# Performance work log

Measured on AMD Instinct MI355X. Metric: run time of the kernel, lower is better.

Reference implementation:

```python
import jax, jax.numpy as jnp
import numpy as np
import itertools

N = 2048
E = 2
B = 8
MAX_ORDERS = (3, 2)
FS = (8, 64, N)  # fs[-1] must equal N for the final Linear (as in the torch code)


def _term_matrices(gsos: np.ndarray, max_order: int) -> np.ndarray:
    """All multigraph polynomial terms S_{i1} @ ... @ S_{id}, d = 1..max_order.
    gsos: [E, N, N] -> returns [T, N, N] with T = E + E^2 + ... + E^max_order."""
    terms = []
    for length in range(1, max_order + 1):
        for idxs in itertools.product(range(gsos.shape[0]), repeat=length):
            m = gsos[idxs[0]]
            for j in idxs[1:]:
                m = m @ gsos[j]
            terms.append(m)
    return np.stack(terms, axis=0)


def setup_inputs() -> dict:
    rng = np.random.default_rng(0)
    # scale so products of up to 3 GSOs stay bounded (op-norm of randn/sqrt(N) ~ 2)
    gsos = (rng.standard_normal((E, N, N)) / (2.0 * np.sqrt(N))).astype(np.float32)
    terms1 = jnp.asarray(_term_matrices(gsos, MAX_ORDERS[0]))  # [14, N, N]
    terms2 = jnp.asarray(_term_matrices(gsos, MAX_ORDERS[1]))  # [6,  N, N]

    key = jax.random.key(0)
    k_x, k_w1, k_w2, k_lin = jax.random.split(key, 4)
    x = jax.random.normal(k_x, (B, FS[0], N), dtype=jnp.float32)
    # torch init: normal(mean=0.05, std=0.01); f_edge dim (=1) squeezed
    w1 = 0.05 + 0.01 * jax.random.normal(k_w1, (FS[1], terms1.shape[0] + 1, FS[0]), dtype=jnp.float32)
    b1 = jnp.zeros((FS[1], 1), dtype=jnp.float32)
    w2 = 0.05 + 0.01 * jax.random.normal(k_w2, (FS[2], terms2.shape[0] + 1, FS[1]), dtype=jnp.float32)
    b2 = jnp.zeros((FS[2], 1), dtype=jnp.float32)
    w_lin = jax.random.normal(k_lin, (2, N), dtype=jnp.float32) / np.sqrt(N)
    b_lin = jnp.zeros((2,), dtype=jnp.float32)
    return dict(x=x, terms1=terms1, terms2=terms2, w1=w1, b1=b1, w2=w2, b2=b2,
                w_lin=w_lin, b_lin=b_lin)


def _mg_filter(x, terms, w, b):
    """MultiGraphFilter forward (f_edge=1 squeezed).
    x: [B,G,N], terms: [T,N,N], w: [F,T+1,G], b: [F,1] -> [B,F,N].
    Equivalent to the torch repeat+matmul+cat+contract, without replication."""
    xS = jnp.einsum('bgm,tmn->btgn', x, terms)          # diffusion for every term
    z = jnp.concatenate([x[:, None], xS], axis=1)        # [B, K=T+1, G, N] (k=0 identity)
    return jnp.einsum('bkgn,fkg->bfn', z, w) + b         # combine + bias


def reference(x, terms1, terms2, w1, b1, w2, b2, w_lin, b_lin):
    h = jax.nn.sigmoid(_mg_filter(x, terms1, w1, b1))    # [B, 64,  N]
    h = jax.nn.sigmoid(_mg_filter(h, terms2, w2, b2))    # [B, N,   N]
    # torch nn.Linear(fs[-1]=N, 2) acts on the last (node) dim
    y = jax.nn.sigmoid(jnp.einsum('bfn,on->bfo', h, w_lin) + b_lin)  # [B, N, 2]
    return jnp.abs(y)
```

## Files before the change

kernel.cpp:

```cpp
#include <hip/hip_runtime.h>

typedef __attribute__((ext_vector_type(8))) short short8;
typedef __attribute__((ext_vector_type(4))) float f32x4;
typedef __attribute__((ext_vector_type(4))) unsigned short u16x4;

#define NN 2048
#define KG2 448
#define NK1 15
#define NG1 8
#define NF1 64
#define SLICE (2048L * 2048L)
#define XSL (64L * 2048L)
#define HSL (512L * 2048L)

static __device__ __forceinline__ unsigned short f2bf(float v) {
    union { float f; unsigned int u; } a; a.f = v;
    unsigned int u = a.u;
    u += 0x7fffu + ((u >> 16) & 1u);
    return (unsigned short)(u >> 16);
}
static __device__ __forceinline__ float bf2f(unsigned short s) {
    union { float f; unsigned int u; } a; a.u = ((unsigned int)s) << 16;
    return a.f;
}
static __device__ __forceinline__ float sigmoidf_(float v) {
    return 1.f / (1.f + __expf(-v));
}
template <int N> static __device__ __forceinline__ void waitvm() {
    asm volatile("s_waitcnt vmcnt(%0)" ::"n"(N) : "memory");
}
template <int LPT> static __device__ __forceinline__ void waitrem(int rem) {
    if (rem >= 3) waitvm<3 * LPT>();
    else if (rem == 2) waitvm<2 * LPT>();
    else if (rem == 1) waitvm<1 * LPT>();
    else waitvm<0>();
}

template <int BM, int BN, int PIPE>
static __device__ __forceinline__ void gemm_core(
    const unsigned short* __restrict__ Ap, int lda,
    const unsigned short* __restrict__ Bp, int ldb, int K,
    unsigned short* Alds, unsigned short* Blds,
    f32x4 (&acc)[BM / 32][BN / 32], int tid) {
    constexpr int MI = BM / 32, NI = BN / 32;
    constexpr int ACH = BM / 64, BCH = BN / 64;
    constexpr int LPT = ACH + BCH;
    const int lane = tid & 63;
    const int wv = tid >> 6;
    const int q = lane >> 4, r = lane & 15;
    const int wm = (wv >> 1) * (BM / 2), wn = (wv & 1) * (BN / 2);

    auto stage = [&](int k0, int buf) {
        unsigned short* Ab = Alds + buf * (BM * 32);
        unsigned short* Bb = Blds + buf * (BN * 32);
#pragma unroll
        for (int c = 0; c < ACH; ++c) {
            const int row = (tid >> 2) + c * 64;
            const unsigned short* gp = Ap + (long)row * lda + k0 + (tid & 3) * 8;
            char* lb = (char*)Ab + c * 4096 + wv * 1024;
            __builtin_amdgcn_global_load_lds(
                (const __attribute__((address_space(1))) void*)gp,
                (__attribute__((address_space(3))) void*)lb, 16, 0, 0);
        }
#pragma unroll
        for (int c = 0; c < BCH; ++c) {
            const int row = (tid >> 2) + c * 64;
            const unsigned short* gp = Bp + (long)row * ldb + k0 + (tid & 3) * 8;
            char* lb = (char*)Bb + c * 4096 + wv * 1024;
            __builtin_amdgcn_global_load_lds(
                (const __attribute__((address_space(1))) void*)gp,
                (__attribute__((address_space(3))) void*)lb, 16, 0, 0);
        }
    };
    auto compute = [&](int buf) {
        const unsigned short* Ab = Alds + buf * (BM * 32);
        const unsigned short* Bb = Blds + buf * (BN * 32);
        short8 af[MI], bfv[NI];
#pragma unroll
        for (int i = 0; i < MI; ++i)
            af[i] = *(const short8*)&Ab[(wm + i * 16 + r) * 32 + q * 8];
#pragma unroll
        for (int j = 0; j < NI; ++j)
            bfv[j] = *(const short8*)&Bb[(wn + j * 16 + r) * 32 + q * 8];
#pragma unroll
        for (int i = 0; i < MI; ++i)
#pragma unroll
            for (int j = 0; j < NI; ++j)
                acc[i][j] = __builtin_amdgcn_mfma_f32_16x16x32_bf16(
                    af[i], bfv[j], acc[i][j], 0, 0, 0);
    };

    const int NT = K >> 5;
    if constexpr (PIPE == 1) {
        for (int t = 0; t < NT; ++t) {
            stage(t * 32, 0);
            __syncthreads();
            compute(0);
            __syncthreads();
        }
    } else {
#pragma unroll
        for (int p = 0; p < PIPE - 1; ++p)
            if (p < NT) stage(p * 32, p);
        for (int t = 0; t < NT; ++t) {
            if (t + PIPE - 1 < NT)
                stage((t + PIPE - 1) * 32, (t + PIPE - 1) & (PIPE - 1));
            int rem = NT - 1 - t;
            if (rem > PIPE - 1) rem = PIPE - 1;
            waitrem<LPT>(rem);
            __builtin_amdgcn_s_barrier();
            compute(t & (PIPE - 1));
            __builtin_amdgcn_s_barrier();
        }
    }
}

template <int BM, int BN>
static __device__ __forceinline__ void epi_bf16(
    f32x4 (&acc)[BM / 32][BN / 32], unsigned short* dst, int ld, int tid) {
    const int lane = tid & 63, wv = tid >> 6, q = lane >> 4, r = lane & 15;
    const int wm = (wv >> 1) * (BM / 2), wn = (wv & 1) * (BN / 2);
#pragma unroll
    for (int i = 0; i < BM / 32; ++i)
#pragma unroll
        for (int j = 0; j < BN / 32; ++j)
#pragma unroll
            for (int e = 0; e < 4; ++e)
                dst[(long)(wm + i * 16 + q * 4 + e) * ld + wn + j * 16 + r] =
                    f2bf(acc[i][j][e]);
}

template <int BM, int BN>
static __device__ __forceinline__ void epi_z2t(
    f32x4 (&acc)[BM / 32][BN / 32], unsigned short* z2t,
    int m0, int n0, int kidx, int tid) {
    const int lane = tid & 63, wv = tid >> 6, q = lane >> 4, r = lane & 15;
    const int wm = (wv >> 1) * (BM / 2), wn = (wv & 1) * (BN / 2);
#pragma unroll
    for (int i = 0; i < BM / 32; ++i)
#pragma unroll
        for (int j = 0; j < BN / 32; ++j) {
            const int row0 = m0 + wm + i * 16 + q * 4;
            const int bb = row0 >> 6, gg = row0 & 63;
            const int col = n0 + wn + j * 16 + r;
            u16x4 pk;
            pk[0] = f2bf(acc[i][j][0]); pk[1] = f2bf(acc[i][j][1]);
            pk[2] = f2bf(acc[i][j][2]); pk[3] = f2bf(acc[i][j][3]);
            *(u16x4*)&z2t[((long)bb * NN + col) * KG2 + kidx * 64 + gg] = pk;
        }
}

__global__ __launch_bounds__(256) void prep_k(const float* __restrict__ S,
                                              const float* __restrict__ x,
                                              unsigned short* __restrict__ St,
                                              unsigned short* __restrict__ xbf) {
    if (blockIdx.z < 2) {
        __shared__ float t[32][33];
        const int e = blockIdx.z;
        const int n0 = blockIdx.x * 32, k0 = blockIdx.y * 32;
        const int tx = threadIdx.x & 31, ty = threadIdx.x >> 5;
        const float* src = S + (long)e * SLICE;
        unsigned short* dst = St + (long)e * SLICE;
#pragma unroll
        for (int i = 0; i < 4; ++i)
            t[ty + i * 8][tx] = src[(long)(k0 + ty + i * 8) * NN + n0 + tx];
        __syncthreads();
#pragma unroll
        for (int i = 0; i < 4; ++i)
            dst[(long)(n0 + ty + i * 8) * NN + k0 + tx] = f2bf(t[tx][ty + i * 8]);
    } else {
        const long i = (long)(blockIdx.y * 64 + blockIdx.x) * 256 + threadIdx.x;
        if (i < 131072L) xbf[i] = f2bf(x[i]);
    }
}

template <int PIPE>
__global__ __launch_bounds__(256) void g1_k(const unsigned short* __restrict__ A,
                                            long a_bstride, int a_shr,
                                            const unsigned short* __restrict__ St,
                                            unsigned short* __restrict__ outp) {
    __shared__ __attribute__((aligned(16))) unsigned short smem[PIPE * 128 * 32];
    const int tid = threadIdx.x;
    const int n0 = blockIdx.x * 64;
    const int z = blockIdx.z;
    const unsigned short* Ap = A + (long)(z >> a_shr) * a_bstride;
    const unsigned short* Bp = St + (long)(z & 1) * SLICE + (long)n0 * NN;

    f32x4 acc[2][2];
#pragma unroll
    for (int i = 0; i < 2; ++i)
#pragma unroll
        for (int j = 0; j < 2; ++j) acc[i][j] = (f32x4){0.f, 0.f, 0.f, 0.f};
    gemm_core<64, 64, PIPE>(Ap, NN, Bp, NN, NN, smem, smem + PIPE * 64 * 32,
                            acc, tid);
    epi_bf16<64, 64>(acc, outp + (long)z * XSL + n0, NN, tid);
}

template <int PIPE, bool CHAIN>
__global__ __launch_bounds__(256) void g2_k(const unsigned short* __restrict__ A,
                                            long a_bstride, int a_shr,
                                            const unsigned short* __restrict__ St,
                                            unsigned short* __restrict__ z2t,
                                            int kbase,
                                            unsigned short* __restrict__ chain) {
    __shared__ __attribute__((aligned(16))) unsigned short smem[PIPE * 192 * 32];
    const int tid = threadIdx.x;
    const int n0 = blockIdx.x * 128;
    const int m0 = blockIdx.y * 64;
    const int z = blockIdx.z;
    const unsigned short* Ap = A + (long)(z >> a_shr) * a_bstride + (long)m0 * NN;
    const unsigned short* Bp = St + (long)(z & 1) * SLICE + (long)n0 * NN;

    f32x4 acc[2][4];
#pragma unroll
    for (int i = 0; i < 2; ++i)
#pragma unroll
        for (int j = 0; j < 4; ++j) acc[i][j] = (f32x4){0.f, 0.f, 0.f, 0.f};
    gemm_core<64, 128, PIPE>(Ap, NN, Bp, NN, NN, smem, smem + PIPE * 64 * 32,
                             acc, tid);
    epi_z2t<64, 128>(acc, z2t, m0, n0, kbase + z, tid);
    if (CHAIN)
        epi_bf16<64, 128>(acc, chain + (long)z * HSL + (long)m0 * NN + n0, NN, tid);
}

__global__ __launch_bounds__(256) void combine1_k(const float* __restrict__ x,
                                                  const unsigned short* __restrict__ xSbf,
                                                  const float* __restrict__ w1,
                                                  const float* __restrict__ b1,
                                                  const float* __restrict__ w2,
                                                  unsigned short* __restrict__ A2,
                                                  unsigned short* __restrict__ z2t,
                                                  unsigned short* __restrict__ w2bf) {
    const int tid = threadIdx.x;
    if (blockIdx.y >= 8) {
        const int sb = (blockIdx.y - 8) * 16 + blockIdx.x;
        for (long i4 = (long)sb * 256 + tid; i4 < 229376L; i4 += 32768L) {
            const float4 v = *(const float4*)&w2[i4 * 4];
            u16x4 pk;
            pk[0] = f2bf(v.x); pk[1] = f2bf(v.y);
            pk[2] = f2bf(v.z); pk[3] = f2bf(v.w);
            *(u16x4*)&w2bf[i4 * 4] = pk;
        }
        return;
    }
    __shared__ float w1s[NF1 * NK1 * NG1];
    for (int i = tid; i < NF1 * NK1 * NG1; i += 256) w1s[i] = w1[i];
    __syncthreads();

    const int b = blockIdx.y;
    const int n = blockIdx.x * 128 + (tid & 127);
    const int fh = tid >> 7;

    float accv[32];
#pragma unroll
    for (int f = 0; f < 32; ++f) accv[f] = 0.f;

    for (int k = 0; k < NK1; ++k) {
        float vv[NG1];
#pragma unroll
        for (int g = 0; g < NG1; ++g) {
            if (k == 0) vv[g] = x[(long)(b * 8 + g) * NN + n];
            else vv[g] = bf2f(xSbf[(long)(k - 1) * XSL + (long)(b * 8 + g) * NN + n]);
        }
#pragma unroll
        for (int f = 0; f < 32; ++f) {
            const float* wp = &w1s[((fh * 32 + f) * NK1 + k) * NG1];
            float s = 0.f;
#pragma unroll
            for (int g = 0; g < NG1; ++g) s += vv[g] * wp[g];
            accv[f] += s;
        }
    }
    unsigned short hb[32];
#pragma unroll
    for (int f = 0; f < 32; ++f) {
        const int fg = fh * 32 + f;
        const float h = sigmoidf_(accv[f] + b1[fg]);
        hb[f] = f2bf(h);
        A2[(long)(b * 64 + fg) * NN + n] = hb[f];
    }
    const long zb = ((long)(b * NN + n)) * KG2 + fh * 32;
#pragma unroll
    for (int c = 0; c < 4; ++c) {
        short8 v;
#pragma unroll
        for (int jj = 0; jj < 8; ++jj) v[jj] = (short)hb[c * 8 + jj];
        *(short8*)&z2t[zb + c * 8] = v;
    }
}

__global__ __launch_bounds__(512, 4) void g3_k(
    const unsigned short* __restrict__ w2bf,
    const unsigned short* __restrict__ z2t,
    const float* __restrict__ b2, const float* __restrict__ wlin,
    float* __restrict__ partial) {
    __shared__ __attribute__((aligned(16))) unsigned short Asm[128 * 64];
    __shared__ __attribute__((aligned(16))) unsigned short Bsm[256 * 64];
    __shared__ float ored[128][2];
    const int tid = threadIdx.x;
    const int bid = blockIdx.x;
    const int xcd = bid & 7, j = bid >> 3;
    const int np = xcd * 8 + (j >> 4);
    const int n0 = np * 256;
    const int m0 = (j & 15) * 128;
    const int lane = tid & 63, wv = tid >> 6;
    const int q = lane >> 4, r = lane & 15;
    const int wm = (wv >> 2) * 64, wn = (wv & 3) * 64;
    const int qs = (tid & 7) ^ ((tid >> 3) & 7);
    const int rx = r & 7;

    const unsigned short* Ap = w2bf + (long)m0 * KG2;
    const unsigned short* Bp = z2t + (long)n0 * KG2;

    f32x4 acc[4][4];
#pragma unroll
    for (int i = 0; i < 4; ++i)
#pragma unroll
        for (int j2 = 0; j2 < 4; ++j2) acc[i][j2] = (f32x4){0.f, 0.f, 0.f, 0.f};

    for (int t = 0; t < 7; ++t) {
        const int k0 = t * 64;
#pragma unroll
        for (int c = 0; c < 2; ++c) {
            const int row = (tid >> 3) + c * 64;
            const unsigned short* gp = Ap + (long)row * KG2 + k0 + qs * 8;
            char* lb = (char*)Asm + c * 8192 + wv * 1024;
            __builtin_amdgcn_global_load_lds(
                (const __attribute__((address_space(1))) void*)gp,
                (__attribute__((address_space(3))) void*)lb, 16, 0, 0);
        }
#pragma unroll
        for (int c = 0; c < 4; ++c) {
            const int row = (tid >> 3) + c * 64;
            const unsigned short* gp = Bp + (long)row * KG2 + k0 + qs * 8;
            char* lb = (char*)Bsm + c * 8192 + wv * 1024;
            __builtin_amdgcn_global_load_lds(
                (const __attribute__((address_space(1))) void*)gp,
                (__attribute__((address_space(3))) void*)lb, 16, 0, 0);
        }
        __syncthreads();
#pragma unroll
        for (int kk = 0; kk < 2; ++kk) {
            short8 af[4], bfv[4];
#pragma unroll
            for (int i = 0; i < 4; ++i)
                af[i] = *(const short8*)&Asm[(wm + i * 16 + r) * 64 +
                                             (((kk * 4 + q) ^ rx) * 8)];
#pragma unroll
            for (int j2 = 0; j2 < 4; ++j2)
                bfv[j2] = *(const short8*)&Bsm[(wn + j2 * 16 + r) * 64 +
                                               (((kk * 4 + q) ^ rx) * 8)];
#pragma unroll
            for (int i = 0; i < 4; ++i)
#pragma unroll
                for (int j2 = 0; j2 < 4; ++j2)
                    acc[i][j2] = __builtin_amdgcn_mfma_f32_16x16x32_bf16(
                        af[i], bfv[j2], acc[i][j2], 0, 0, 0);
        }
        __syncthreads();
    }

    if (tid < 128) { ored[tid][0] = 0.f; ored[tid][1] = 0.f; }
    __syncthreads();
    float wl0[4], wl1[4];
#pragma unroll
    for (int j2 = 0; j2 < 4; ++j2) {
        const int nn = (n0 + wn + j2 * 16 + r) & (NN - 1);
        wl0[j2] = wlin[nn];
        wl1[j2] = wlin[NN + nn];
    }
#pragma unroll
    for (int i = 0; i < 4; ++i) {
#pragma unroll
        for (int e = 0; e < 4; ++e) {
            const int lrow = wm + i * 16 + q * 4 + e;
            const float bs = b2[m0 + lrow];
            float p0 = 0.f, p1 = 0.f;
#pragma unroll
            for (int j2 = 0; j2 < 4; ++j2) {
                const float s = sigmoidf_(acc[i][j2][e] + bs);
                p0 += s * wl0[j2];
                p1 += s * wl1[j2];
            }
#pragma unroll
            for (int mk = 1; mk < 16; mk <<= 1) {
                p0 += __shfl_xor(p0, mk);
                p1 += __shfl_xor(p1, mk);
            }
            if (r == 0) {
                atomicAdd(&ored[lrow][0], p0);
                atomicAdd(&ored[lrow][1], p1);
            }
        }
    }
    __syncthreads();
    float* pp = partial + ((long)np * NN + m0) * 2;
    if (tid < 128) {
        pp[tid * 2 + 0] = ored[tid][0];
        pp[tid * 2 + 1] = ored[tid][1];
    }
}

__global__ __launch_bounds__(256) void finish_k(const float* __restrict__ partial,
                                                const float* __restrict__ blin,
                                                float* __restrict__ out) {
    const int i = blockIdx.x * 256 + threadIdx.x;
    if (i >= 32768) return;
    const int b = i >> 12;
    const int fo = i & 4095;
    float s = 0.f;
#pragma unroll
    for (int p = 0; p < 8; ++p)
        s += partial[(long)(b * 8 + p) * 4096 + fo];
    out[i] = fabsf(sigmoidf_(s + blin[i & 1]));
}

extern "C" void kernel_launch(void* const* d_in, const int* in_sizes, int n_in,
                              void* d_out, int out_size, void* d_ws, size_t ws_size,
                              hipStream_t stream) {
    const float* x      = (const float*)d_in[0];
    const float* terms1 = (const float*)d_in[1];
    const float* w1     = (const float*)d_in[3];
    const float* b1     = (const float*)d_in[4];
    const float* w2     = (const float*)d_in[5];
    const float* b2     = (const float*)d_in[6];
    const float* wlin   = (const float*)d_in[7];
    const float* blin   = (const float*)d_in[8];
    float* out = (float*)d_out;

    char* ws = (char*)d_ws;
    unsigned short* xbf   = (unsigned short*)(ws + 0);
    unsigned short* w2bf  = (unsigned short*)(ws + 262144);
    unsigned short* St    = (unsigned short*)(ws + 2097152);
    unsigned short* xSbf  = (unsigned short*)(ws + 18874368);
    unsigned short* A2    = (unsigned short*)(ws + 22544384);
    unsigned short* hS1bf = (unsigned short*)(ws + 24641536);
    unsigned short* z2t   = (unsigned short*)(ws + 28835840);
    float*          part  = (float*)(ws + 43515904);

    prep_k<<<dim3(64, 64, 3), 256, 0, stream>>>(terms1, x, St, xbf);

    g1_k<4><<<dim3(32, 1, 2), 256, 0, stream>>>(xbf, 0L, 30, St, xSbf);
    g1_k<4><<<dim3(32, 1, 4), 256, 0, stream>>>(xSbf, XSL, 1, St, xSbf + 2 * XSL);
    g1_k<4><<<dim3(32, 1, 8), 256, 0, stream>>>(xSbf + 2 * XSL, XSL, 1, St,
                                                xSbf + 6 * XSL);

    combine1_k<<<dim3(16, 16), 256, 0, stream>>>(x, xSbf, w1, b1, w2, A2, z2t,
                                                 w2bf);

    g2_k<4, true><<<dim3(16, 8, 2), 256, 0, stream>>>(A2, 0L, 30, St, z2t, 1,
                                                      hS1bf);
    g2_k<4, false><<<dim3(16, 8, 4), 256, 0, stream>>>(hS1bf, HSL, 1, St, z2t, 3,
                                                       nullptr);

    g3_k<<<1024, 512, 0, stream>>>(w2bf, z2t, b2, wlin, part);
    finish_k<<<128, 256, 0, stream>>>(part, blin, out);
}
```

Baseline: 181.6 us.

## Double-buffer g3_k LDS tiles and overlap next-tile loads with MFMA

The g3_k GEMM now uses two LDS buffers for the A and B tiles. It issues global-to-LDS loads for the next K tile while the current tile is being consumed, with the B prefetch split to sit between the two k-halves. Raw s_barrier plus vmcnt waits replace the __syncthreads pairs, and setprio is raised around the MFMA bursts. LDS use doubles and the occupancy hint of 4 blocks is dropped, so fewer blocks may fit per CU. The kernel is only one part of the pipeline.

Result: slower. 197.3 us (+8.6%).

```diff
diff --git a/kernel.cpp b/kernel.cpp
--- a/kernel.cpp
+++ b/kernel.cpp
@@ -289,13 +289,13 @@
     }
 }
 
-__global__ __launch_bounds__(512, 4) void g3_k(
+__global__ __launch_bounds__(512) void g3_k(
     const unsigned short* __restrict__ w2bf,
     const unsigned short* __restrict__ z2t,
     const float* __restrict__ b2, const float* __restrict__ wlin,
     float* __restrict__ partial) {
-    __shared__ __attribute__((aligned(16))) unsigned short Asm[128 * 64];
-    __shared__ __attribute__((aligned(16))) unsigned short Bsm[256 * 64];
+    __shared__ __attribute__((aligned(16))) unsigned short Asm[2][128 * 64];
+    __shared__ __attribute__((aligned(16))) unsigned short Bsm[2][256 * 64];
     __shared__ float ored[128][2];
     const int tid = threadIdx.x;
     const int bid = blockIdx.x;
@@ -312,52 +312,91 @@
     const unsigned short* Ap = w2bf + (long)m0 * KG2;
     const unsigned short* Bp = z2t + (long)n0 * KG2;
 
-    f32x4 acc[4][4];
-#pragma unroll
-    for (int i = 0; i < 4; ++i)
-#pragma unroll
-        for (int j2 = 0; j2 < 4; ++j2) acc[i][j2] = (f32x4){0.f, 0.f, 0.f, 0.f};
-
-    for (int t = 0; t < 7; ++t) {
+    auto stageA = [&](int t, int buf) {
         const int k0 = t * 64;
 #pragma unroll
         for (int c = 0; c < 2; ++c) {
             const int row = (tid >> 3) + c * 64;
             const unsigned short* gp = Ap + (long)row * KG2 + k0 + qs * 8;
-            char* lb = (char*)Asm + c * 8192 + wv * 1024;
+            char* lb = (char*)(&Asm[buf][0]) + c * 8192 + wv * 1024;
             __builtin_amdgcn_global_load_lds(
                 (const __attribute__((address_space(1))) void*)gp,
                 (__attribute__((address_space(3))) void*)lb, 16, 0, 0);
         }
+    };
+    auto stageB = [&](int t, int buf) {
+        const int k0 = t * 64;
 #pragma unroll
         for (int c = 0; c < 4; ++c) {
             const int row = (tid >> 3) + c * 64;
             const unsigned short* gp = Bp + (long)row * KG2 + k0 + qs * 8;
-            char* lb = (char*)Bsm + c * 8192 + wv * 1024;
+            char* lb = (char*)(&Bsm[buf][0]) + c * 8192 + wv * 1024;
             __builtin_amdgcn_global_load_lds(
                 (const __attribute__((address_space(1))) void*)gp,
                 (__attribute__((address_space(3))) void*)lb, 16, 0, 0);
         }
-        __syncthreads();
-#pragma unroll
-        for (int kk = 0; kk < 2; ++kk) {
+    };
+
+    f32x4 acc[4][4];
+#pragma unroll
+    for (int i = 0; i < 4; ++i)
+#pragma unroll
+        for (int j2 = 0; j2 < 4; ++j2) acc[i][j2] = (f32x4){0.f, 0.f, 0.f, 0.f};
+
+    stageA(0, 0);
+    stageB(0, 0);
+    for (int t = 0; t < 7; ++t) {
+        const int buf = t & 1;
+        if (t < 6) {
+            stageA(t + 1, buf ^ 1);
+            waitvm<2>();
+        } else {
+            waitvm<0>();
+        }
+        __builtin_amdgcn_s_barrier();
+        asm volatile("" ::: "memory");
+        {
             short8 af[4], bfv[4];
 #pragma unroll
             for (int i = 0; i < 4; ++i)
-                af[i] = *(const short8*)&Asm[(wm + i * 16 + r) * 64 +
-                                             (((kk * 4 + q) ^ rx) * 8)];
+                af[i] = *(const short8*)&Asm[buf][(wm + i * 16 + r) * 64 +
+                                                  ((q ^ rx) * 8)];
 #pragma unroll
             for (int j2 = 0; j2 < 4; ++j2)
-                bfv[j2] = *(const short8*)&Bsm[(wn + j2 * 16 + r) * 64 +
-                                               (((kk * 4 + q) ^ rx) * 8)];
+                bfv[j2] = *(const short8*)&Bsm[buf][(wn + j2 * 16 + r) * 64 +
+                                                    ((q ^ rx) * 8)];
+            __builtin_amdgcn_s_setprio(1);
 #pragma unroll
             for (int i = 0; i < 4; ++i)
 #pragma unroll
                 for (int j2 = 0; j2 < 4; ++j2)
                     acc[i][j2] = __builtin_amdgcn_mfma_f32_16x16x32_bf16(
                         af[i], bfv[j2], acc[i][j2], 0, 0, 0);
-        }
-        __syncthreads();
+            __builtin_amdgcn_s_setprio(0);
+        }
+        if (t < 6) stageB(t + 1, buf ^ 1);
+        {
+            short8 af[4], bfv[4];
+#pragma unroll
+            for (int i = 0; i < 4; ++i)
+                af[i] = *(const short8*)&Asm[buf][(wm + i * 16 + r) * 64 +
+                                                  (((4 + q) ^ rx) * 8)];
+#pragma unroll
+            for (int j2 = 0; j2 < 4; ++j2)
+                bfv[j2] = *(const short8*)&Bsm[buf][(wn + j2 * 16 + r) * 64 +
+                                                    (((4 + q) ^ rx) * 8)];
+            __builtin_amdgcn_s_setprio(1);
+#pragma unroll
+            for (int i = 0; i < 4; ++i)
+#pragma unroll
+                for (int j2 = 0; j2 < 4; ++j2)
+                    acc[i][j2] = __builtin_amdgcn_mfma_f32_16x16x32_bf16(
+                        af[i], bfv[j2], acc[i][j2], 0, 0, 0);
+            __builtin_amdgcn_s_setprio(0);
+        }
+        asm volatile("" ::: "memory");
+        __builtin_amdgcn_s_barrier();
+        asm volatile("" ::: "memory");
     }
 
     if (tid < 128) { ored[tid][0] = 0.f; ored[tid][1] = 0.f; }
```
